# Performance work log

Measured on AMD Instinct MI355X. Metric: run time of the kernel, lower is better.

Reference implementation:

```python
import jax, jax.numpy as jnp
import numpy as np

B, N, DK, DV = 16, 4096, 64, 64


def setup_inputs() -> dict:
    key = jax.random.key(0)
    kq, kk, kv = jax.random.split(key, 3)
    q = jax.random.normal(kq, (B, N, DK), dtype=jnp.float32)
    k = jax.random.normal(kk, (B, N, DK), dtype=jnp.float32)
    v = jax.random.normal(kv, (B, N, DV), dtype=jnp.float32)
    # causal mask: positions j<=i are attendable (mask==True)
    mask = jnp.tril(jnp.ones((N, N), dtype=bool))[None, :, :]  # (1, N, N)
    return {"q": q, "k": k, "v": v, "mask": mask}


def reference(q, k, v, mask):
    # scores: (B, N, N)
    scale = 1.0 / jnp.sqrt(jnp.asarray(q.shape[-1], dtype=q.dtype))
    scores = jnp.einsum('bnd,bmd->bnm', q, k) * scale
    scores = jnp.where(mask, scores, jnp.asarray(-jnp.inf, dtype=scores.dtype))
    attn = jax.nn.softmax(scores, axis=-1)
    # dropout is identity in eval/reference mode
    return jnp.einsum('bnm,bmd->bnd', attn, v)
```

## Files before the change

### kernel.cpp

```cpp
#include <hip/hip_runtime.h>


#define N_SEQ 4096
#define DIM   64

typedef __bf16  bf16x8 __attribute__((ext_vector_type(8)));
typedef unsigned short u16x8 __attribute__((ext_vector_type(8)));
typedef float   f32x4  __attribute__((ext_vector_type(4)));
typedef short   short4v __attribute__((ext_vector_type(4)));

__device__ int g_qcount[8];

static __device__ __forceinline__ unsigned short f2bf(float f) {
    unsigned int u = __float_as_uint(f);
    u += 0x7FFFu + ((u >> 16) & 1u);
    return (unsigned short)(u >> 16);
}

static __device__ __forceinline__ unsigned int pk2bf(float a, float b) {
#if defined(__HIP_DEVICE_COMPILE__) && __has_builtin(__builtin_amdgcn_cvt_pk_bf16_f32)
    typedef __bf16 bf16x2_t __attribute__((ext_vector_type(2)));
    bf16x2_t r = __builtin_amdgcn_cvt_pk_bf16_f32(a, b);
    return __builtin_bit_cast(unsigned int, r);
#else
    return (unsigned int)f2bf(a) | ((unsigned int)f2bf(b) << 16);
#endif
}

static __device__ __forceinline__ float fexp2(float x) {
#if defined(__HIP_DEVICE_COMPILE__) && __has_builtin(__builtin_amdgcn_exp2f)
    return __builtin_amdgcn_exp2f(x);
#else
    return exp2f(x);
#endif
}

static __device__ __forceinline__ bf16x8 ld_frag(const void* p) {
    u16x8 u = *reinterpret_cast<const u16x8*>(p);
    return __builtin_bit_cast(bf16x8, u);
}

static __device__ __forceinline__ f32x4 mfma_pv(uint2 a, uint2 b, f32x4 c) {
#if defined(__HIP_DEVICE_COMPILE__)
#if __has_builtin(__builtin_amdgcn_mfma_f32_16x16x16bf16_1k)
    return __builtin_amdgcn_mfma_f32_16x16x16bf16_1k(
        __builtin_bit_cast(short4v, a), __builtin_bit_cast(short4v, b), c, 0, 0, 0);
#else
    f32x4 d;
    asm volatile("v_mfma_f32_16x16x16_bf16 %0, %1, %2, %3"
                 : "=v"(d) : "v"(a), "v"(b), "v"(c));
    return d;
#endif
#else
    (void)a; (void)b;
    return c;
#endif
}

static __device__ __forceinline__ void gl_lds16(const unsigned short* g, unsigned short* l) {
#if defined(__HIP_DEVICE_COMPILE__)
    __builtin_amdgcn_global_load_lds(
        (const __attribute__((address_space(1))) unsigned int*)(g),
        (__attribute__((address_space(3))) unsigned int*)(l), 16, 0, 0);
#else
    (void)g; (void)l;
#endif
}

__global__ __launch_bounds__(256)
void prep_kv(const float* __restrict__ K, const float* __restrict__ V,
             unsigned short* __restrict__ wsK, unsigned short* __restrict__ wsV) {
    if (blockIdx.x == 0 && blockIdx.y == 0 && blockIdx.z == 0 && threadIdx.x < 8)
        g_qcount[threadIdx.x] = 0;
    const int b = blockIdx.y, t = blockIdx.x;
    if (blockIdx.z == 0) {
        const float* src = K + ((size_t)b * N_SEQ + t * 64) * DIM;
        unsigned short* dst = wsK + ((size_t)(b * 64 + t)) * 4096;
        #pragma unroll
        for (int ph = 0; ph < 2; ++ph) {
            const int gidx = threadIdx.x + ph * 256;
            const int r = gidx >> 3, g = gidx & 7;
            const float* p = src + r * DIM + g * 8;
            f32x4 f0 = *reinterpret_cast<const f32x4*>(p);
            f32x4 f1 = *reinterpret_cast<const f32x4*>(p + 4);
            uint4 w;
            w.x = pk2bf(f0[0], f0[1]); w.y = pk2bf(f0[2], f0[3]);
            w.z = pk2bf(f1[0], f1[1]); w.w = pk2bf(f1[2], f1[3]);
            *reinterpret_cast<uint4*>(&dst[(r * 8 + (g ^ (r & 7))) * 8]) = w;
        }
    } else {
        const int dv = threadIdx.x & 63;
        const int g0 = threadIdx.x >> 6;
        const float* src = V + ((size_t)b * N_SEQ + t * 64) * DIM + dv;
        unsigned short* dst = wsV + ((size_t)(b * 64 + t)) * 4096;
        #pragma unroll
        for (int ph = 0; ph < 2; ++ph) {
            const int gp = g0 + ph * 4;
            float p[8];
            #pragma unroll
            for (int e = 0; e < 8; ++e) {
                const int pos = gp * 8 + e;
                const int kp  = ((pos >> 2) & 3) * 16 + (pos >> 4) * 4 + (pos & 3);
                p[e] = src[(size_t)kp * DIM];
            }
            uint4 w;
            w.x = pk2bf(p[0], p[1]); w.y = pk2bf(p[2], p[3]);
            w.z = pk2bf(p[4], p[5]); w.w = pk2bf(p[6], p[7]);
            *reinterpret_cast<uint4*>(&dst[(dv * 8 + (gp ^ (dv & 7))) * 8]) = w;
        }
    }
}

__global__ __launch_bounds__(256)
void attn_fwd(const float* __restrict__ Q, const unsigned short* __restrict__ wsK,
              const unsigned short* __restrict__ wsV, float* __restrict__ O,
              float* __restrict__ wsO, float* __restrict__ wsL) {
    __shared__ unsigned short kbuf[2][4096];
    __shared__ unsigned short vbuf[2][4096];
    __shared__ int s_item;

    const int tid  = threadIdx.x;
    const int wave = tid >> 6;
    const int lane = tid & 63;
    const int quad = lane >> 4;
    const int ln   = lane & 15;
    const int ln7  = lane & 7;
    const int r    = (int)blockIdx.x & 7;

    int kaddr[2][4];
    #pragma unroll
    for (int s = 0; s < 2; ++s)
        #pragma unroll
        for (int nt = 0; nt < 4; ++nt)
            kaddr[s][nt] = (nt * 16 + ln) * 128 + (((s * 4 + quad) ^ ln7) * 16);
    int vaddr[2][4];
    #pragma unroll
    for (int c = 0; c < 2; ++c)
        #pragma unroll
        for (int dvt = 0; dvt < 4; ++dvt)
            vaddr[c][dvt] = (dvt * 16 + ln) * 128 + ((((quad << 1) | c) ^ ln7) * 16);

    const int dma_off = wave * 1024 + lane * 8;
    const uint2 ones  = make_uint2(0x3F803F80u, 0x3F803F80u);
    const float QS = 0.125f * 1.44269504f;

    for (;;) {
        __syncthreads();
        if (tid == 0) s_item = atomicAdd(&g_qcount[r], 1);
        __syncthreads();
        const int item = s_item;
        if (item >= 192) break;

        int tt, b, kt0, kt1, half;
        bool partial;
        if (item < 128) {
            tt   = 63 - (item >> 2);
            b    = r * 2 + ((item >> 1) & 1);
            half = item & 1;
            const int d  = tt + 1;
            const int h0 = (d + 1) >> 1;
            kt0 = half ? h0 : 0;
            kt1 = half ? d  : h0;
            partial = true;
        } else {
            const int i2 = item - 128;
            tt   = 31 - (i2 >> 1);
            b    = r * 2 + (i2 & 1);
            half = 0;
            kt0  = 0;
            kt1  = tt + 1;
            partial = false;
        }
        const int i0   = tt * 64;
        const int qloc = i0 + wave * 16 + ln;

        const float* qptr = Q + ((size_t)b * N_SEQ + i0 + wave * 16 + ln) * DIM;
        u16x8 qa[2];
        #pragma unroll
        for (int s = 0; s < 2; ++s) {
            const float* p = qptr + s * 32 + quad * 8;
            f32x4 f0 = *reinterpret_cast<const f32x4*>(p);
            f32x4 f1 = *reinterpret_cast<const f32x4*>(p + 4);
            #pragma unroll
            for (int jj = 0; jj < 4; ++jj) {
                qa[s][jj]     = f2bf(f0[jj] * QS);
                qa[s][4 + jj] = f2bf(f1[jj] * QS);
            }
        }

        const unsigned short* kt_src = wsK + (size_t)b * 64 * 4096;
        const unsigned short* vt_src = wsV + (size_t)b * 64 * 4096;

        auto dma = [&](int kt, int bufi) {
            const unsigned short* ks = kt_src + (size_t)kt * 4096 + dma_off;
            const unsigned short* vs = vt_src + (size_t)kt * 4096 + dma_off;
            #pragma unroll
            for (int i = 0; i < 2; ++i) {
                gl_lds16(ks + i * 512, &kbuf[bufi][wave * 1024 + i * 512]);
                gl_lds16(vs + i * 512, &vbuf[bufi][wave * 1024 + i * 512]);
            }
        };

        f32x4 o_acc[4] = {};
        f32x4 lacc = {};

        auto compute = [&](int kt, const unsigned short* kb, const unsigned short* vb) {
            f32x4 st[4] = {};
            #pragma unroll
            for (int s = 0; s < 2; ++s) {
                bf16x8 qf = __builtin_bit_cast(bf16x8, qa[s]);
                #pragma unroll
                for (int nt = 0; nt < 4; ++nt) {
                    bf16x8 kf = ld_frag((const char*)kb + kaddr[s][nt]);
                    st[nt] = __builtin_amdgcn_mfma_f32_16x16x32_bf16(kf, qf, st[nt], 0, 0, 0);
                }
            }
            uint2 pk_d[4];
            if (kt == tt) {
                const int kbase = kt * 64 + quad * 4;
                #pragma unroll
                for (int nt = 0; nt < 4; ++nt) {
                    const int kp = kbase + nt * 16;
                    float p0 = fexp2((kp + 0 > qloc) ? -3.0e38f : st[nt][0]);
                    float p1 = fexp2((kp + 1 > qloc) ? -3.0e38f : st[nt][1]);
                    float p2 = fexp2((kp + 2 > qloc) ? -3.0e38f : st[nt][2]);
                    float p3 = fexp2((kp + 3 > qloc) ? -3.0e38f : st[nt][3]);
                    pk_d[nt].x = pk2bf(p0, p1);
                    pk_d[nt].y = pk2bf(p2, p3);
                }
            } else {
                #pragma unroll
                for (int nt = 0; nt < 4; ++nt) {
                    pk_d[nt].x = pk2bf(fexp2(st[nt][0]), fexp2(st[nt][1]));
                    pk_d[nt].y = pk2bf(fexp2(st[nt][2]), fexp2(st[nt][3]));
                }
            }
            #pragma unroll
            for (int c = 0; c < 2; ++c)
                #pragma unroll
                for (int dvt = 0; dvt < 4; ++dvt) {
                    uint4 bv = *reinterpret_cast<const uint4*>(
                        (const char*)vb + vaddr[c][dvt]);
                    o_acc[dvt] = mfma_pv(pk_d[2 * c],     make_uint2(bv.x, bv.y), o_acc[dvt]);
                    o_acc[dvt] = mfma_pv(pk_d[2 * c + 1], make_uint2(bv.z, bv.w), o_acc[dvt]);
                }
            #pragma unroll
            for (int nt = 0; nt < 4; ++nt)
                lacc = mfma_pv(pk_d[nt], ones, lacc);
        };

        dma(kt0, 0);
        int kt = kt0, bufi = 0;
        while (true) {
            __syncthreads();
            if (kt + 1 < kt1) dma(kt + 1, bufi ^ 1);
            compute(kt, kbuf[bufi], vbuf[bufi]);
            if (++kt == kt1) break;
            bufi ^= 1;
        }

        if (!partial) {
            float* obase = O + ((size_t)b * N_SEQ + i0 + wave * 16) * DIM;
            #pragma unroll
            for (int rr = 0; rr < 4; ++rr) {
                const float inv = 1.0f / lacc[rr];
                #pragma unroll
                for (int dvt = 0; dvt < 4; ++dvt)
                    obase[(quad * 4 + rr) * DIM + dvt * 16 + ln] = o_acc[dvt][rr] * inv;
            }
        } else {
            float* po = wsO + (((size_t)(b * 32 + (tt - 32)) * 2 + half) * 4096)
                      + (wave * 16) * 64;
            float* pl = wsL + (((size_t)(b * 32 + (tt - 32)) * 2 + half) * 64)
                      + wave * 16;
            #pragma unroll
            for (int rr = 0; rr < 4; ++rr) {
                #pragma unroll
                for (int dvt = 0; dvt < 4; ++dvt)
                    po[(quad * 4 + rr) * 64 + dvt * 16 + ln] = o_acc[dvt][rr];
                if (ln == 0) pl[quad * 4 + rr] = lacc[rr];
            }
        }
    }
}

__global__ __launch_bounds__(256)
void norm_out(const float* __restrict__ wsO, const float* __restrict__ wsL,
              float* __restrict__ O) {
    const int t = 32 + blockIdx.x, b = blockIdx.y;
    const int row = threadIdx.x >> 2;
    const int c0  = (threadIdx.x & 3) * 16;
    const size_t base = (size_t)(b * 32 + (t - 32)) * 2;
    const float* p0 = wsO + base * 4096 + row * 64 + c0;
    const float* p1 = p0 + 4096;
    const float* l  = wsL + base * 64;
    const float inv = 1.0f / (l[row] + l[64 + row]);
    float* o = O + ((size_t)b * N_SEQ + t * 64 + row) * 64 + c0;
    #pragma unroll
    for (int i = 0; i < 16; i += 4) {
        f32x4 a = *reinterpret_cast<const f32x4*>(p0 + i);
        f32x4 c = *reinterpret_cast<const f32x4*>(p1 + i);
        f32x4 v = (a + c) * inv;
        *reinterpret_cast<f32x4*>(o + i) = v;
    }
}

extern "C" void kernel_launch(void* const* d_in, const int* in_sizes, int n_in,
                              void* d_out, int out_size, void* d_ws, size_t ws_size,
                              hipStream_t stream) {
    const float* q = (const float*)d_in[0];
    const float* k = (const float*)d_in[1];
    const float* v = (const float*)d_in[2];
    float* out = (float*)d_out;

    unsigned short* wsK = (unsigned short*)d_ws;
    unsigned short* wsV = wsK + (size_t)16 * 64 * 4096;
    float* wsO = (float*)(wsV + (size_t)16 * 64 * 4096);
    float* wsL = wsO + (size_t)16 * 32 * 2 * 4096;

    prep_kv<<<dim3(64, 16, 2), dim3(256), 0, stream>>>(k, v, wsK, wsV);
    attn_fwd<<<dim3(1024), dim3(256), 0, stream>>>(q, wsK, wsV, out, wsO, wsL);
    norm_out<<<dim3(32, 16), dim3(256), 0, stream>>>(wsO, wsL, out);
}
```

Measured before the change: 202.8 us.

## Replace atomic work queue with static balanced per-block work assignment

```diff
diff --git a/kernel.cpp b/kernel.cpp
--- a/kernel.cpp
+++ b/kernel.cpp
@@ -8,8 +8,6 @@
 typedef unsigned short u16x8 __attribute__((ext_vector_type(8)));
 typedef float   f32x4  __attribute__((ext_vector_type(4)));
 typedef short   short4v __attribute__((ext_vector_type(4)));
-
-__device__ int g_qcount[8];
 
 static __device__ __forceinline__ unsigned short f2bf(float f) {
     unsigned int u = __float_as_uint(f);
@@ -70,8 +68,6 @@
 __global__ __launch_bounds__(256)
 void prep_kv(const float* __restrict__ K, const float* __restrict__ V,
              unsigned short* __restrict__ wsK, unsigned short* __restrict__ wsV) {
-    if (blockIdx.x == 0 && blockIdx.y == 0 && blockIdx.z == 0 && threadIdx.x < 8)
-        g_qcount[threadIdx.x] = 0;
     const int b = blockIdx.y, t = blockIdx.x;
     if (blockIdx.z == 0) {
         const float* src = K + ((size_t)b * N_SEQ + t * 64) * DIM;
@@ -117,7 +113,6 @@
               float* __restrict__ wsO, float* __restrict__ wsL) {
     __shared__ unsigned short kbuf[2][4096];
     __shared__ unsigned short vbuf[2][4096];
-    __shared__ int s_item;
 
     const int tid  = threadIdx.x;
     const int wave = tid >> 6;
@@ -125,7 +120,25 @@
     const int quad = lane >> 4;
     const int ln   = lane & 15;
     const int ln7  = lane & 7;
-    const int r    = (int)blockIdx.x & 7;
+
+    const int L    = (int)blockIdx.x;
+    const int r    = L & 7;
+    const int w    = L >> 3;
+    const int role = w & 1;
+    const int bsel = (w >> 1) & 1;
+    const int j    = w >> 2;
+    const int b    = r * 2 + bsel;
+    const int T    = 63 - j;
+
+    int it_tile[2], it_k0[2], it_k1[2], it_half[2], n_items;
+    if (role == 0) {
+        it_tile[0] = j;  it_k0[0] = 0; it_k1[0] = j + 1;  it_half[0] = -1;
+        it_tile[1] = T;  it_k0[1] = 0; it_k1[1] = 31 - j; it_half[1] = 0;
+        n_items = 2;
+    } else {
+        it_tile[0] = T;  it_k0[0] = 31 - j; it_k1[0] = 64 - j; it_half[0] = 1;
+        n_items = 1;
+    }
 
     int kaddr[2][4];
     #pragma unroll
@@ -144,122 +157,104 @@
     const uint2 ones  = make_uint2(0x3F803F80u, 0x3F803F80u);
     const float QS = 0.125f * 1.44269504f;
 
-    for (;;) {
-        __syncthreads();
-        if (tid == 0) s_item = atomicAdd(&g_qcount[r], 1);
-        __syncthreads();
-        const int item = s_item;
-        if (item >= 192) break;
-
-        int tt, b, kt0, kt1, half;
-        bool partial;
-        if (item < 128) {
-            tt   = 63 - (item >> 2);
-            b    = r * 2 + ((item >> 1) & 1);
-            half = item & 1;
-            const int d  = tt + 1;
-            const int h0 = (d + 1) >> 1;
-            kt0 = half ? h0 : 0;
-            kt1 = half ? d  : h0;
-            partial = true;
-        } else {
-            const int i2 = item - 128;
-            tt   = 31 - (i2 >> 1);
-            b    = r * 2 + (i2 & 1);
-            half = 0;
-            kt0  = 0;
-            kt1  = tt + 1;
-            partial = false;
-        }
+    const unsigned short* kt_src = wsK + (size_t)b * 64 * 4096;
+    const unsigned short* vt_src = wsV + (size_t)b * 64 * 4096;
+
+    for (int it = 0; it < n_items; ++it) {
+        const int tt   = it_tile[it];
+        const int kt0  = it_k0[it];
+        const int kt1  = it_k1[it];
+        const int half = it_half[it];
         const int i0   = tt * 64;
         const int qloc = i0 + wave * 16 + ln;
 
-        const float* qptr = Q + ((size_t)b * N_SEQ + i0 + wave * 16 + ln) * DIM;
-        u16x8 qa[2];
-        #pragma unroll
-        for (int s = 0; s < 2; ++s) {
-            const float* p = qptr + s * 32 + quad * 8;
-            f32x4 f0 = *reinterpret_cast<const f32x4*>(p);
-            f32x4 f1 = *reinterpret_cast<const f32x4*>(p + 4);
-            #pragma unroll
-            for (int jj = 0; jj < 4; ++jj) {
-                qa[s][jj]     = f2bf(f0[jj] * QS);
-                qa[s][4 + jj] = f2bf(f1[jj] * QS);
-            }
-        }
-
-        const unsigned short* kt_src = wsK + (size_t)b * 64 * 4096;
-        const unsigned short* vt_src = wsV + (size_t)b * 64 * 4096;
-
-        auto dma = [&](int kt, int bufi) {
-            const unsigned short* ks = kt_src + (size_t)kt * 4096 + dma_off;
-            const unsigned short* vs = vt_src + (size_t)kt * 4096 + dma_off;
-            #pragma unroll
-            for (int i = 0; i < 2; ++i) {
-                gl_lds16(ks + i * 512, &kbuf[bufi][wave * 1024 + i * 512]);
-                gl_lds16(vs + i * 512, &vbuf[bufi][wave * 1024 + i * 512]);
-            }
-        };
+        __syncthreads();
 
         f32x4 o_acc[4] = {};
         f32x4 lacc = {};
 
-        auto compute = [&](int kt, const unsigned short* kb, const unsigned short* vb) {
-            f32x4 st[4] = {};
+        if (kt0 < kt1) {
+            const float* qptr = Q + ((size_t)b * N_SEQ + i0 + wave * 16 + ln) * DIM;
+            u16x8 qa[2];
             #pragma unroll
             for (int s = 0; s < 2; ++s) {
-                bf16x8 qf = __builtin_bit_cast(bf16x8, qa[s]);
-                #pragma unroll
-                for (int nt = 0; nt < 4; ++nt) {
-                    bf16x8 kf = ld_frag((const char*)kb + kaddr[s][nt]);
-                    st[nt] = __builtin_amdgcn_mfma_f32_16x16x32_bf16(kf, qf, st[nt], 0, 0, 0);
+                const float* p = qptr + s * 32 + quad * 8;
+                f32x4 f0 = *reinterpret_cast<const f32x4*>(p);
+                f32x4 f1 = *reinterpret_cast<const f32x4*>(p + 4);
+                #pragma unroll
+                for (int jj = 0; jj < 4; ++jj) {
+                    qa[s][jj]     = f2bf(f0[jj] * QS);
+                    qa[s][4 + jj] = f2bf(f1[jj] * QS);
                 }
             }
-            uint2 pk_d[4];
-            if (kt == tt) {
-                const int kbase = kt * 64 + quad * 4;
-                #pragma unroll
-                for (int nt = 0; nt < 4; ++nt) {
-                    const int kp = kbase + nt * 16;
-                    float p0 = fexp2((kp + 0 > qloc) ? -3.0e38f : st[nt][0]);
-                    float p1 = fexp2((kp + 1 > qloc) ? -3.0e38f : st[nt][1]);
-                    float p2 = fexp2((kp + 2 > qloc) ? -3.0e38f : st[nt][2]);
-                    float p3 = fexp2((kp + 3 > qloc) ? -3.0e38f : st[nt][3]);
-                    pk_d[nt].x = pk2bf(p0, p1);
-                    pk_d[nt].y = pk2bf(p2, p3);
+
+            auto dma = [&](int kt, int bufi) {
+                const unsigned short* ks = kt_src + (size_t)kt * 4096 + dma_off;
+                const unsigned short* vs = vt_src + (size_t)kt * 4096 + dma_off;
+                #pragma unroll
+                for (int i = 0; i < 2; ++i) {
+                    gl_lds16(ks + i * 512, &kbuf[bufi][wave * 1024 + i * 512]);
+                    gl_lds16(vs + i * 512, &vbuf[bufi][wave * 1024 + i * 512]);
                 }
-            } else {
-                #pragma unroll
-                for (int nt = 0; nt < 4; ++nt) {
-                    pk_d[nt].x = pk2bf(fexp2(st[nt][0]), fexp2(st[nt][1]));
-                    pk_d[nt].y = pk2bf(fexp2(st[nt][2]), fexp2(st[nt][3]));
+            };
+
+            auto compute = [&](int kt, const unsigned short* kb, const unsigned short* vb) {
+                f32x4 st[4] = {};
+                #pragma unroll
+                for (int s = 0; s < 2; ++s) {
+                    bf16x8 qf = __builtin_bit_cast(bf16x8, qa[s]);
+                    #pragma unroll
+                    for (int nt = 0; nt < 4; ++nt) {
+                        bf16x8 kf = ld_frag((const char*)kb + kaddr[s][nt]);
+                        st[nt] = __builtin_amdgcn_mfma_f32_16x16x32_bf16(kf, qf, st[nt], 0, 0, 0);
+                    }
                 }
-            }
-            #pragma unroll
-            for (int c = 0; c < 2; ++c)
-                #pragma unroll
-                for (int dvt = 0; dvt < 4; ++dvt) {
-                    uint4 bv = *reinterpret_cast<const uint4*>(
-                        (const char*)vb + vaddr[c][dvt]);
-                    o_acc[dvt] = mfma_pv(pk_d[2 * c],     make_uint2(bv.x, bv.y), o_acc[dvt]);
-                    o_acc[dvt] = mfma_pv(pk_d[2 * c + 1], make_uint2(bv.z, bv.w), o_acc[dvt]);
+                uint2 pk_d[4];
+                if (kt == tt) {
+                    const int kbase = kt * 64 + quad * 4;
+                    #pragma unroll
+                    for (int nt = 0; nt < 4; ++nt) {
+                        const int kp = kbase + nt * 16;
+                        float p0 = fexp2((kp + 0 > qloc) ? -3.0e38f : st[nt][0]);
+                        float p1 = fexp2((kp + 1 > qloc) ? -3.0e38f : st[nt][1]);
+                        float p2 = fexp2((kp + 2 > qloc) ? -3.0e38f : st[nt][2]);
+                        float p3 = fexp2((kp + 3 > qloc) ? -3.0e38f : st[nt][3]);
+                        pk_d[nt].x = pk2bf(p0, p1);
+                        pk_d[nt].y = pk2bf(p2, p3);
+                    }
+                } else {
+                    #pragma unroll
+                    for (int nt = 0; nt < 4; ++nt) {
+                        pk_d[nt].x = pk2bf(fexp2(st[nt][0]), fexp2(st[nt][1]));
+                        pk_d[nt].y = pk2bf(fexp2(st[nt][2]), fexp2(st[nt][3]));
+                    }
                 }
-            #pragma unroll
-            for (int nt = 0; nt < 4; ++nt)
-                lacc = mfma_pv(pk_d[nt], ones, lacc);
-        };
-
-        dma(kt0, 0);
-        int kt = kt0, bufi = 0;
-        while (true) {
-            __syncthreads();
-            if (kt + 1 < kt1) dma(kt + 1, bufi ^ 1);
-            compute(kt, kbuf[bufi], vbuf[bufi]);
-            if (++kt == kt1) break;
-            bufi ^= 1;
+                #pragma unroll
+                for (int c = 0; c < 2; ++c)
+                    #pragma unroll
+                    for (int dvt = 0; dvt < 4; ++dvt) {
+                        uint4 bv = *reinterpret_cast<const uint4*>(
+                            (const char*)vb + vaddr[c][dvt]);
+                        o_acc[dvt] = mfma_pv(pk_d[2 * c],     make_uint2(bv.x, bv.y), o_acc[dvt]);
+                        o_acc[dvt] = mfma_pv(pk_d[2 * c + 1], make_uint2(bv.z, bv.w), o_acc[dvt]);
+                    }
+                #pragma unroll
+                for (int nt = 0; nt < 4; ++nt)
+                    lacc = mfma_pv(pk_d[nt], ones, lacc);
+            };
+
+            dma(kt0, 0);
+            int kt = kt0, bufi = 0;
+            while (true) {
+                __syncthreads();
+                if (kt + 1 < kt1) dma(kt + 1, bufi ^ 1);
+                compute(kt, kbuf[bufi], vbuf[bufi]);
+                if (++kt == kt1) break;
+                bufi ^= 1;
+            }
         }
 
-        if (!partial) {
+        if (half < 0) {
             float* obase = O + ((size_t)b * N_SEQ + i0 + wave * 16) * DIM;
             #pragma unroll
             for (int rr = 0; rr < 4; ++rr) {
```

New measurement: 194.2 us. 1.04x faster.
